# Optimization experiments

Measured on AMD Instinct MI355X. Metric: run time of the kernel, lower is better.

Reference implementation:

```python
import jax, jax.numpy as jnp
import numpy as np

N = 131072  # time steps
D = 4       # SDE state dimension


def setup_inputs() -> dict:
    key = jax.random.key(0)
    k = jax.random.split(key, 6)
    F = 0.1 * jax.random.normal(k[0], (D, D), jnp.float32)  # only shape/dtype used by filter
    H = jnp.zeros((1, D), jnp.float32).at[0, 0].set(1.0)    # observe first state component
    P_inf = jnp.eye(D, dtype=jnp.float32)
    # stable per-step transitions: spectral radius ~0.9
    A_seq = 0.9 * jnp.eye(D, dtype=jnp.float32)[None] + 0.02 * jax.random.normal(k[1], (N, D, D), jnp.float32)
    # PSD process noise per step
    S = 0.05 * jax.random.normal(k[2], (N, D, D), jnp.float32)
    Q_seq = jnp.einsum('nij,nkj->nik', S, S) + 1e-3 * jnp.eye(D, dtype=jnp.float32)[None]
    residual = jax.random.normal(k[3], (N,), jnp.float32)   # y - mean_fn(times)
    mask = jnp.ones((N,), jnp.float32)                      # all steps observed
    R_seq = 0.1 + 0.05 * jax.random.uniform(k[4], (N,), jnp.float32)  # noise_var + floor
    return dict(F=F, H=H, P_inf=P_inf, A_seq=A_seq, Q_seq=Q_seq,
                residual=residual, mask=mask, R_seq=R_seq)


def _kalman_filter(F, H, P_inf, A_seq, Q_seq, residual, mask, R_seq):
    d = F.shape[0]
    eye = jnp.eye(d, dtype=F.dtype)
    h = H[0]  # (d,)
    log_2pi = jnp.log(2.0 * jnp.pi).astype(F.dtype)

    def step(carry, inputs):
        m, P = carry
        A, Q, r_n, mask_n, R_n = inputs
        m_pred = A @ m
        P_pred = A @ P @ A.T + Q
        P_pred = 0.5 * (P_pred + P_pred.T)
        Ph = P_pred @ h                 # (d,)
        S = h @ Ph + R_n                # innovation variance
        innov = r_n - h @ m_pred
        is_obs = mask_n == 1
        S_safe = jnp.where(is_obs, S, 1.0)
        K = jnp.where(is_obs, Ph / S_safe, jnp.zeros_like(Ph))
        m_new = m_pred + K * innov
        I_KH = eye - K[:, None] * h[None, :]
        P_new = I_KH @ P_pred @ I_KH.T + R_n * (K[:, None] * K[None, :])
        P_new = 0.5 * (P_new + P_new.T)
        ll = jnp.where(is_obs, -0.5 * (log_2pi + jnp.log(S_safe) + innov * innov / S_safe), 0.0)
        return (m_new, P_new), (m_pred, P_pred, m_new, P_new, ll)

    m0 = jnp.zeros(d, dtype=F.dtype)
    _, (m_pred_seq, P_pred_seq, m_filt_seq, P_filt_seq, ll_seq) = jax.lax.scan(
        step, (m0, P_inf), (A_seq, Q_seq, residual, mask, R_seq))
    return m_pred_seq, P_pred_seq, m_filt_seq, P_filt_seq, jnp.sum(ll_seq)


def _rts_smoother(m_pred_seq, P_pred_seq, m_filt_seq, P_filt_seq, A_seq):
    def step(carry, inputs):
        m_ns, P_ns = carry
        m_f, P_f, m_pn, P_pn, A_n = inputs
        J = jnp.linalg.solve(P_pn.T, A_n @ P_f.T).T
        m_s = m_f + J @ (m_ns - m_pn)
        P_s = P_f + J @ (P_ns - P_pn) @ J.T
        P_s = 0.5 * (P_s + P_s.T)
        return (m_s, P_s), (m_s, P_s)

    m_T = m_filt_seq[-1]
    P_T = P_filt_seq[-1]
    inputs = (m_filt_seq[:-1], P_filt_seq[:-1], m_pred_seq[1:], P_pred_seq[1:], A_seq[1:])
    _, (m_s, P_s) = jax.lax.scan(step, (m_T, P_T), inputs, reverse=True)
    return (jnp.concatenate([m_s, m_T[None]], axis=0),
            jnp.concatenate([P_s, P_T[None]], axis=0))


def reference(F, H, P_inf, A_seq, Q_seq, residual, mask, R_seq):
    m_pred, P_pred, m_filt, P_filt, log_marginal = _kalman_filter(
        F, H, P_inf, A_seq, Q_seq, residual, mask, R_seq)
    m_smooth, P_smooth = _rts_smoother(m_pred, P_pred, m_filt, P_filt, A_seq)
    h = H[0]
    means = m_smooth @ h                                   # (N,) observation-space means
    vars_ = jnp.einsum('i,nij,j->n', h, P_smooth, h)       # (N,) marginal variances
    return means, vars_, log_marginal
```

## Files before the change

### kernel.cpp

```cpp
#include <hip/hip_runtime.h>
#include <math.h>

#define NN 131072
#define WUP 32
#define TPB 256
#define NBLK (NN / TPB)
#define WINF (TPB + WUP + 1)
#define WINB (TPB + WUP - 1)
#define LOG2PI 1.8378770664093453f

typedef __attribute__((ext_vector_type(2))) float f2;

__device__ float4 g_f[5][NN];
__device__ float4 g_J[4][NN];
__device__ float4 g_W0[NN];
__device__ float4 g_W1[NN];
__device__ float2 g_W2[NN];
__device__ float4 g_u[NN];
__device__ double g_llb[NBLK];

__device__ __forceinline__ f2 bc(float s) {
  f2 r = {s, s};
  return r;
}
#define PF(a, b, c) __builtin_elementwise_fma((a), (b), (c))

template <int E>
__device__ __forceinline__ void ldpk(const float4 (*s)[E], int w, f2* M) {
#pragma unroll
  for (int c = 0; c < 4; ++c) {
    float4 v = s[c][w];
    M[2 * c] = f2{v.x, v.y};
    M[2 * c + 1] = f2{v.z, v.w};
  }
}

__device__ __forceinline__ void sym_rows(const float4 t0, const float4 t1, const float2 t2,
                                         f2* M) {
  M[0] = f2{t0.x, t0.y};
  M[1] = f2{t0.z, t0.w};
  M[2] = f2{t0.y, t1.x};
  M[3] = f2{t1.y, t1.z};
  M[4] = f2{t0.z, t1.y};
  M[5] = f2{t1.w, t2.x};
  M[6] = f2{t0.w, t1.z};
  M[7] = f2{t2.x, t2.y};
}

__device__ __forceinline__ void kf_step_pk(const f2* __restrict__ AT, const f2* __restrict__ Q,
                                           float r, float mk, float R, f2* __restrict__ m,
                                           f2* __restrict__ P, float& Ss, float& innov,
                                           bool& obs) {
  float m0 = m[0][0], m1 = m[0][1], m2_ = m[1][0], m3 = m[1][1];
  f2 mp[2];
#pragma unroll
  for (int p = 0; p < 2; ++p) {
    f2 acc = AT[p] * bc(m0);
    acc = PF(bc(m1), AT[2 + p], acc);
    acc = PF(bc(m2_), AT[4 + p], acc);
    acc = PF(bc(m3), AT[6 + p], acc);
    mp[p] = acc;
  }

  f2 T[8];
#pragma unroll
  for (int i = 0; i < 4; ++i) {
    float a0 = AT[0 + (i >> 1)][i & 1];
    float a1 = AT[2 + (i >> 1)][i & 1];
    float a2 = AT[4 + (i >> 1)][i & 1];
    float a3 = AT[6 + (i >> 1)][i & 1];
#pragma unroll
    for (int p = 0; p < 2; ++p) {
      f2 acc = P[p] * bc(a0);
      acc = PF(bc(a1), P[2 + p], acc);
      acc = PF(bc(a2), P[4 + p], acc);
      acc = PF(bc(a3), P[6 + p], acc);
      T[2 * i + p] = acc;
    }
  }

  f2 Pp[8];
#pragma unroll
  for (int i = 0; i < 4; ++i) {
    float t0 = T[2 * i][0], t1 = T[2 * i][1], t2 = T[2 * i + 1][0], t3 = T[2 * i + 1][1];
#pragma unroll
    for (int p = 0; p < 2; ++p) {
      f2 acc = PF(bc(t0), AT[p], Q[2 * i + p]);
      acc = PF(bc(t1), AT[2 + p], acc);
      acc = PF(bc(t2), AT[4 + p], acc);
      acc = PF(bc(t3), AT[6 + p], acc);
      Pp[2 * i + p] = acc;
    }
  }

  float S = Pp[0][0] + R;
  innov = r - mp[0][0];
  obs = (mk == 1.0f);
  Ss = obs ? S : 1.0f;
  float kf = obs ? __builtin_amdgcn_rcpf(S) : 0.0f;
  f2 K[2] = {Pp[0] * bc(kf), Pp[1] * bc(kf)};
#pragma unroll
  for (int p = 0; p < 2; ++p) m[p] = PF(K[p], bc(innov), mp[p]);

#pragma unroll
  for (int i = 0; i < 4; ++i) {
    float Ki = K[i >> 1][i & 1];
#pragma unroll
    for (int p = 0; p < 2; ++p) P[2 * i + p] = PF(bc(-Ki), Pp[p], Pp[2 * i + p]);
  }
}

__device__ __forceinline__ void chol_solve_pk(const f2* __restrict__ S, const f2* __restrict__ T,
                                              f2* __restrict__ X) {
  float s00 = S[0][0];
  float s10 = S[2][0], s11 = S[2][1];
  float s20 = S[4][0], s21 = S[4][1], s22 = S[5][0];
  float s30 = S[6][0], s31 = S[6][1], s32 = S[7][0], s33 = S[7][1];
  float i00 = __builtin_amdgcn_rsqf(s00);
  float l10 = s10 * i00, l20 = s20 * i00, l30 = s30 * i00;
  float i11 = __builtin_amdgcn_rsqf(s11 - l10 * l10);
  float l21 = (s21 - l20 * l10) * i11;
  float l31 = (s31 - l30 * l10) * i11;
  float i22 = __builtin_amdgcn_rsqf(s22 - l20 * l20 - l21 * l21);
  float l32 = (s32 - l30 * l20 - l31 * l21) * i22;
  float i33 = __builtin_amdgcn_rsqf(s33 - l30 * l30 - l31 * l31 - l32 * l32);
#pragma unroll
  for (int c = 0; c < 4; ++c) {
    float t0 = T[0 + (c >> 1)][c & 1];
    float t1 = T[2 + (c >> 1)][c & 1];
    float t2 = T[4 + (c >> 1)][c & 1];
    float t3 = T[6 + (c >> 1)][c & 1];
    float y0 = t0 * i00;
    float y1 = (t1 - l10 * y0) * i11;
    float y2 = (t2 - l20 * y0 - l21 * y1) * i22;
    float y3 = (t3 - l30 * y0 - l31 * y1 - l32 * y2) * i33;
    float x3 = y3 * i33;
    float x2 = (y2 - l32 * x3) * i22;
    float x1 = (y1 - l21 * x2 - l31 * x3) * i11;
    float x0 = (y0 - l10 * x1 - l20 * x2 - l30 * x3) * i00;
    X[0 + (c >> 1)][c & 1] = x0;
    X[2 + (c >> 1)][c & 1] = x1;
    X[4 + (c >> 1)][c & 1] = x2;
    X[6 + (c >> 1)][c & 1] = x3;
  }
}

__device__ __forceinline__ void make_record_pk(int n, const f2* __restrict__ m,
                                               const f2* __restrict__ P,
                                               const f2* __restrict__ AT,
                                               const f2* __restrict__ Q) {
  float m0 = m[0][0], m1 = m[0][1], m2_ = m[1][0], m3 = m[1][1];
  f2 pm[2];
#pragma unroll
  for (int p = 0; p < 2; ++p) {
    f2 acc = AT[p] * bc(m0);
    acc = PF(bc(m1), AT[2 + p], acc);
    acc = PF(bc(m2_), AT[4 + p], acc);
    acc = PF(bc(m3), AT[6 + p], acc);
    pm[p] = acc;
  }

  f2 T[8];
#pragma unroll
  for (int i = 0; i < 4; ++i) {
    float a0 = AT[0 + (i >> 1)][i & 1];
    float a1 = AT[2 + (i >> 1)][i & 1];
    float a2 = AT[4 + (i >> 1)][i & 1];
    float a3 = AT[6 + (i >> 1)][i & 1];
#pragma unroll
    for (int p = 0; p < 2; ++p) {
      f2 acc = P[p] * bc(a0);
      acc = PF(bc(a1), P[2 + p], acc);
      acc = PF(bc(a2), P[4 + p], acc);
      acc = PF(bc(a3), P[6 + p], acc);
      T[2 * i + p] = acc;
    }
  }

  f2 Ppn[8];
#pragma unroll
  for (int i = 0; i < 4; ++i) {
    float t0 = T[2 * i][0], t1 = T[2 * i][1], t2 = T[2 * i + 1][0], t3 = T[2 * i + 1][1];
#pragma unroll
    for (int p = 0; p < 2; ++p) {
      f2 acc = PF(bc(t0), AT[p], Q[2 * i + p]);
      acc = PF(bc(t1), AT[2 + p], acc);
      acc = PF(bc(t2), AT[4 + p], acc);
      acc = PF(bc(t3), AT[6 + p], acc);
      Ppn[2 * i + p] = acc;
    }
  }

  f2 X[8];
  chol_solve_pk(Ppn, T, X);

  float p0 = pm[0][0], p1 = pm[0][1], p2 = pm[1][0], p3 = pm[1][1];
  f2 u[2];
#pragma unroll
  for (int p = 0; p < 2; ++p) {
    f2 acc = X[p] * bc(p0);
    acc = PF(bc(p1), X[2 + p], acc);
    acc = PF(bc(p2), X[4 + p], acc);
    acc = PF(bc(p3), X[6 + p], acc);
    u[p] = m[p] - acc;
  }

  f2 Jp[8];
#pragma unroll
  for (int i = 0; i < 4; ++i) {
    float x0 = X[0 + (i >> 1)][i & 1];
    float x1 = X[2 + (i >> 1)][i & 1];
    float x2 = X[4 + (i >> 1)][i & 1];
    float x3 = X[6 + (i >> 1)][i & 1];
#pragma unroll
    for (int p = 0; p < 2; ++p) {
      f2 acc = Ppn[p] * bc(x0);
      acc = PF(bc(x1), Ppn[2 + p], acc);
      acc = PF(bc(x2), Ppn[4 + p], acc);
      acc = PF(bc(x3), Ppn[6 + p], acc);
      Jp[2 * i + p] = acc;
    }
  }
  f2 W[8];
#pragma unroll
  for (int i = 0; i < 4; ++i) {
    float j0 = Jp[2 * i][0], j1 = Jp[2 * i][1], j2 = Jp[2 * i + 1][0], j3 = Jp[2 * i + 1][1];
#pragma unroll
    for (int p = 0; p < 2; ++p) {
      f2 acc = X[p] * bc(j0);
      acc = PF(bc(j1), X[2 + p], acc);
      acc = PF(bc(j2), X[4 + p], acc);
      acc = PF(bc(j3), X[6 + p], acc);
      W[2 * i + p] = P[2 * i + p] - acc;
    }
  }

#pragma unroll
  for (int i = 0; i < 4; ++i)
    g_J[i][n] = make_float4(X[0 + (i >> 1)][i & 1], X[2 + (i >> 1)][i & 1],
                            X[4 + (i >> 1)][i & 1], X[6 + (i >> 1)][i & 1]);
  g_W0[n] = make_float4(W[0][0], W[0][1], W[1][0], W[1][1]);
  g_W1[n] = make_float4(W[2][1], W[3][0], W[3][1], W[5][0]);
  g_W2[n] = make_float2(W[5][1], W[7][1]);
  g_u[n] = make_float4(u[0][0], u[0][1], u[1][0], u[1][1]);
}

__global__ __launch_bounds__(TPB, 1) void fwd_kernel(const float* __restrict__ P_inf,
                                                     const float* __restrict__ A_seq,
                                                     const float* __restrict__ Q_seq,
                                                     const float* __restrict__ residual,
                                                     const float* __restrict__ mask,
                                                     const float* __restrict__ R_seq) {
  __shared__ float4 sAT[4][WINF];
  __shared__ float4 sQ0[WINF], sQ1[WINF];
  __shared__ float2 sQ2[WINF];
  __shared__ float4 sRM[WINF];
  __shared__ double sh[TPB];

  const int B = blockIdx.x * TPB;
  const int base = B - WUP;
  const float4* Af4 = (const float4*)A_seq;
  const float4* Qf4 = (const float4*)Q_seq;
  for (int f = threadIdx.x; f < WINF * 4; f += TPB) {
    int w = f >> 2, c = f & 3;
    int k = base + w;
    k = k < 0 ? 0 : (k > NN - 1 ? NN - 1 : k);
    float4 rowA = Af4[(size_t)k * 4 + c];
    ((float*)&sAT[0][w])[c] = rowA.x;
    ((float*)&sAT[1][w])[c] = rowA.y;
    ((float*)&sAT[2][w])[c] = rowA.z;
    ((float*)&sAT[3][w])[c] = rowA.w;
    float4 rowQ = Qf4[(size_t)k * 4 + c];
    if (c == 0) {
      sQ0[w] = rowQ;
    } else if (c == 1) {
      sQ1[w].x = rowQ.y;
      sQ1[w].y = rowQ.z;
      sQ1[w].z = rowQ.w;
    } else if (c == 2) {
      sQ1[w].w = rowQ.z;
      sQ2[w].x = rowQ.w;
    } else {
      sQ2[w].y = rowQ.w;
    }
  }
  for (int w = threadIdx.x; w < WINF; w += TPB) {
    int k = base + w;
    k = k < 0 ? 0 : (k > NN - 1 ? NN - 1 : k);
    sRM[w] = make_float4(residual[k], R_seq[k], mask[k], 0.f);
  }
  __syncthreads();

  const int t = threadIdx.x;
  const int n = B + t;
  int s0 = n - WUP;
  if (s0 < 0) s0 = 0;

  f2 m[2] = {f2{0.f, 0.f}, f2{0.f, 0.f}};
  f2 P[8];
#pragma unroll
  for (int i = 0; i < 4; ++i) {
    P[2 * i] = f2{P_inf[i * 4 + 0], P_inf[i * 4 + 1]};
    P[2 * i + 1] = f2{P_inf[i * 4 + 2], P_inf[i * 4 + 3]};
  }

  float Ss = 1.f, innov = 0.f;
  bool obs = false;
#pragma unroll 2
  for (int k = s0; k <= n; ++k) {
    int w = k - base;
    f2 AT[8], Q[8];
    ldpk<WINF>(sAT, w, AT);
    sym_rows(sQ0[w], sQ1[w], sQ2[w], Q);
    float4 rm = sRM[w];
    kf_step_pk(AT, Q, rm.x, rm.z, rm.y, m, P, Ss, innov, obs);
  }

#pragma unroll
  for (int c = 0; c < 4; ++c)
    g_f[c][n] = make_float4(P[2 * c][0], P[2 * c][1], P[2 * c + 1][0], P[2 * c + 1][1]);
  g_f[4][n] = make_float4(m[0][0], m[0][1], m[1][0], m[1][1]);

  if (n < NN - 1) {
    int w = n + 1 - base;
    f2 AT[8], Q[8];
    ldpk<WINF>(sAT, w, AT);
    sym_rows(sQ0[w], sQ1[w], sQ2[w], Q);
    make_record_pk(n, m, P, AT, Q);
  }

  sh[t] = obs ? (double)(-0.5f * (LOG2PI + logf(Ss) + innov * innov / Ss)) : 0.0;
  __syncthreads();
#pragma unroll
  for (int w = TPB / 2; w > 0; w >>= 1) {
    if (t < w) sh[t] += sh[t + w];
    __syncthreads();
  }
  if (t == 0) g_llb[blockIdx.x] = sh[0];
}

__global__ __launch_bounds__(TPB, 1) void bwd_kernel(float* __restrict__ out) {
  __shared__ float4 sJ[4][WINB];
  __shared__ float4 sW0[WINB], sW1[WINB];
  __shared__ float2 sW2[WINB];
  __shared__ float4 su[WINB];
  __shared__ double shd[TPB];

  const int B = blockIdx.x * TPB;
  const int t = threadIdx.x;
  const int n = B + t;
  int e = n + WUP;
  if (e > NN - 1) e = NN - 1;

  f2 Pi[8], mi[2];
#pragma unroll
  for (int c = 0; c < 4; ++c) {
    float4 v = g_f[c][e];
    Pi[2 * c] = f2{v.x, v.y};
    Pi[2 * c + 1] = f2{v.z, v.w};
  }
  {
    float4 v = g_f[4][e];
    mi[0] = f2{v.x, v.y};
    mi[1] = f2{v.z, v.w};
  }

  for (int f = t; f < WINB * 4; f += TPB) {
    int w = f >> 2, c = f & 3;
    int k = B + w;
    if (k > NN - 1) k = NN - 1;
    sJ[c][w] = g_J[c][k];
  }
  for (int w = t; w < WINB; w += TPB) {
    int k = B + w;
    if (k > NN - 1) k = NN - 1;
    sW0[w] = g_W0[k];
    sW1[w] = g_W1[k];
    sW2[w] = g_W2[k];
    su[w] = g_u[k];
  }
  __syncthreads();

  f2 r01 = f2{1.f, 0.f}, r23 = f2{0.f, 0.f};
  float alpha = 0.f, omega = 0.f;
#pragma unroll 2
  for (int k = n; k < e; ++k) {
    int w = k - B;
    float4 j0 = sJ[0][w], j1 = sJ[1][w], j2 = sJ[2][w], j3 = sJ[3][w];
    f2 W[8];
    sym_rows(sW0[w], sW1[w], sW2[w], W);
    float4 uv = su[w];
    float r0 = r01[0], r1 = r01[1], r2 = r23[0], r3 = r23[1];
    alpha += r0 * uv.x + r1 * uv.y + r2 * uv.z + r3 * uv.w;
    f2 s01 = W[0] * bc(r0);
    s01 = PF(bc(r1), W[2], s01);
    s01 = PF(bc(r2), W[4], s01);
    s01 = PF(bc(r3), W[6], s01);
    f2 s23 = W[1] * bc(r0);
    s23 = PF(bc(r1), W[3], s23);
    s23 = PF(bc(r2), W[5], s23);
    s23 = PF(bc(r3), W[7], s23);
    f2 os = r01 * s01;
    os = PF(r23, s23, os);
    omega += os[0] + os[1];
    f2 ja = f2{j0.x, j0.y}, jb = f2{j1.x, j1.y}, jc = f2{j2.x, j2.y}, jd = f2{j3.x, j3.y};
    f2 je = f2{j0.z, j0.w}, jf = f2{j1.z, j1.w}, jg = f2{j2.z, j2.w}, jh = f2{j3.z, j3.w};
    f2 n01 = ja * bc(r0);
    n01 = PF(bc(r1), jb, n01);
    n01 = PF(bc(r2), jc, n01);
    n01 = PF(bc(r3), jd, n01);
    f2 n23 = je * bc(r0);
    n23 = PF(bc(r1), jf, n23);
    n23 = PF(bc(r2), jg, n23);
    n23 = PF(bc(r3), jh, n23);
    r01 = n01;
    r23 = n23;
  }

  {
    float r0 = r01[0], r1 = r01[1], r2 = r23[0], r3 = r23[1];
    float mean = alpha + r0 * mi[0][0] + r1 * mi[0][1] + r2 * mi[1][0] + r3 * mi[1][1];
    f2 s01 = Pi[0] * bc(r0);
    s01 = PF(bc(r1), Pi[2], s01);
    s01 = PF(bc(r2), Pi[4], s01);
    s01 = PF(bc(r3), Pi[6], s01);
    f2 s23 = Pi[1] * bc(r0);
    s23 = PF(bc(r1), Pi[3], s23);
    s23 = PF(bc(r2), Pi[5], s23);
    s23 = PF(bc(r3), Pi[7], s23);
    f2 vs = r01 * s01;
    vs = PF(r23, s23, vs);
    out[n] = mean;
    out[NN + n] = omega + vs[0] + vs[1];
  }

  if (blockIdx.x == 0) {
    double acc = 0.0;
    for (int i = t; i < NBLK; i += TPB) acc += g_llb[i];
    shd[t] = acc;
    __syncthreads();
#pragma unroll
    for (int w = TPB / 2; w > 0; w >>= 1) {
      if (t < w) shd[t] += shd[t + w];
      __syncthreads();
    }
    if (t == 0) out[2 * NN] = (float)shd[0];
  }
}

extern "C" void kernel_launch(void* const* d_in, const int* in_sizes, int n_in, void* d_out,
                              int out_size, void* d_ws, size_t ws_size, hipStream_t stream) {
  const float* P_inf = (const float*)d_in[2];
  const float* A_seq = (const float*)d_in[3];
  const float* Q_seq = (const float*)d_in[4];
  const float* residual = (const float*)d_in[5];
  const float* mask = (const float*)d_in[6];
  const float* R_seq = (const float*)d_in[7];
  float* out = (float*)d_out;

  fwd_kernel<<<NBLK, TPB, 0, stream>>>(P_inf, A_seq, Q_seq, residual, mask, R_seq);
  bwd_kernel<<<NBLK, TPB, 0, stream>>>(out);
}
```

Before: 115.8 us.

## Fuse forward filter and backward smoother into one kernel via shared memory

Merges the forward Kalman filter kernel and the backward RTS smoother kernel into a single kernel. Each block runs 320 threads: 288 compute smoother records (J, W, u) and 256 produce outputs, and records are exchanged through shared memory instead of global arrays. This removes the global round trip for per-step filter state and records and one full kernel boundary. In exchange each block recomputes 32 extra forward records for its backward warm-up window, 64 threads sit idle during the backward phase, and a small separate kernel is added for the log-likelihood reduction.

New measurement: 130.7 us. 12.9% more time.

```diff
diff --git a/kernel.cpp b/kernel.cpp
--- a/kernel.cpp
+++ b/kernel.cpp
@@ -3,20 +3,15 @@
 
 #define NN 131072
 #define WUP 32
-#define TPB 256
-#define NBLK (NN / TPB)
-#define WINF (TPB + WUP + 1)
-#define WINB (TPB + WUP - 1)
+#define TPB 320
+#define NOUT 256
+#define NBLK (NN / NOUT)
+#define WIN 321
+#define NREC 288
 #define LOG2PI 1.8378770664093453f
 
 typedef __attribute__((ext_vector_type(2))) float f2;
 
-__device__ float4 g_f[5][NN];
-__device__ float4 g_J[4][NN];
-__device__ float4 g_W0[NN];
-__device__ float4 g_W1[NN];
-__device__ float2 g_W2[NN];
-__device__ float4 g_u[NN];
 __device__ double g_llb[NBLK];
 
 __device__ __forceinline__ f2 bc(float s) {
@@ -25,11 +20,10 @@
 }
 #define PF(a, b, c) __builtin_elementwise_fma((a), (b), (c))
 
-template <int E>
-__device__ __forceinline__ void ldpk(const float4 (*s)[E], int w, f2* M) {
+__device__ __forceinline__ void ldpk_flat(const float4* s, int stride, int w, f2* M) {
 #pragma unroll
   for (int c = 0; c < 4; ++c) {
-    float4 v = s[c][w];
+    float4 v = s[c * stride + w];
     M[2 * c] = f2{v.x, v.y};
     M[2 * c + 1] = f2{v.z, v.w};
   }
@@ -145,10 +139,11 @@
   }
 }
 
-__device__ __forceinline__ void make_record_pk(int n, const f2* __restrict__ m,
-                                               const f2* __restrict__ P,
-                                               const f2* __restrict__ AT,
-                                               const f2* __restrict__ Q) {
+__device__ __forceinline__ void make_record_reg(const f2* __restrict__ m,
+                                                const f2* __restrict__ P,
+                                                const f2* __restrict__ AT,
+                                                const f2* __restrict__ Q, f2* __restrict__ X,
+                                                f2* __restrict__ W, f2* __restrict__ u) {
   float m0 = m[0][0], m1 = m[0][1], m2_ = m[1][0], m3 = m[1][1];
   f2 pm[2];
 #pragma unroll
@@ -191,11 +186,9 @@
     }
   }
 
-  f2 X[8];
   chol_solve_pk(Ppn, T, X);
 
   float p0 = pm[0][0], p1 = pm[0][1], p2 = pm[1][0], p3 = pm[1][1];
-  f2 u[2];
 #pragma unroll
   for (int p = 0; p < 2; ++p) {
     f2 acc = X[p] * bc(p0);
@@ -221,7 +214,6 @@
       Jp[2 * i + p] = acc;
     }
   }
-  f2 W[8];
 #pragma unroll
   for (int i = 0; i < 4; ++i) {
     float j0 = Jp[2 * i][0], j1 = Jp[2 * i][1], j2 = Jp[2 * i + 1][0], j3 = Jp[2 * i + 1][1];
@@ -234,42 +226,46 @@
       W[2 * i + p] = P[2 * i + p] - acc;
     }
   }
-
-#pragma unroll
-  for (int i = 0; i < 4; ++i)
-    g_J[i][n] = make_float4(X[0 + (i >> 1)][i & 1], X[2 + (i >> 1)][i & 1],
-                            X[4 + (i >> 1)][i & 1], X[6 + (i >> 1)][i & 1]);
-  g_W0[n] = make_float4(W[0][0], W[0][1], W[1][0], W[1][1]);
-  g_W1[n] = make_float4(W[2][1], W[3][0], W[3][1], W[5][0]);
-  g_W2[n] = make_float2(W[5][1], W[7][1]);
-  g_u[n] = make_float4(u[0][0], u[0][1], u[1][0], u[1][1]);
-}
-
-__global__ __launch_bounds__(TPB, 1) void fwd_kernel(const float* __restrict__ P_inf,
-                                                     const float* __restrict__ A_seq,
-                                                     const float* __restrict__ Q_seq,
-                                                     const float* __restrict__ residual,
-                                                     const float* __restrict__ mask,
-                                                     const float* __restrict__ R_seq) {
-  __shared__ float4 sAT[4][WINF];
-  __shared__ float4 sQ0[WINF], sQ1[WINF];
-  __shared__ float2 sQ2[WINF];
-  __shared__ float4 sRM[WINF];
+}
+
+__global__ __launch_bounds__(TPB, 1) void fused_kernel(const float* __restrict__ P_inf,
+                                                       const float* __restrict__ A_seq,
+                                                       const float* __restrict__ Q_seq,
+                                                       const float* __restrict__ residual,
+                                                       const float* __restrict__ mask,
+                                                       const float* __restrict__ R_seq,
+                                                       float* __restrict__ out) {
+  __shared__ __align__(16) char smem[55040];
   __shared__ double sh[TPB];
 
-  const int B = blockIdx.x * TPB;
+  float4* sAT = (float4*)smem;
+  float4* sQ0 = (float4*)(smem + 20544);
+  float4* sQ1 = (float4*)(smem + 25680);
+  float2* sQ2 = (float2*)(smem + 30816);
+  float4* sRM = (float4*)(smem + 33384);
+  float4* rJ = (float4*)smem;
+  float4* rW0 = (float4*)(smem + 18432);
+  float4* rW1 = (float4*)(smem + 23040);
+  float2* rW2 = (float2*)(smem + 27648);
+  float4* ru = (float4*)(smem + 29952);
+  float4* fm = (float4*)(smem + 34560);
+  float4* fP = (float4*)(smem + 38656);
+
+  const int B = blockIdx.x * NOUT;
+  const int t = threadIdx.x;
   const int base = B - WUP;
+
   const float4* Af4 = (const float4*)A_seq;
   const float4* Qf4 = (const float4*)Q_seq;
-  for (int f = threadIdx.x; f < WINF * 4; f += TPB) {
+  for (int f = t; f < WIN * 4; f += TPB) {
     int w = f >> 2, c = f & 3;
     int k = base + w;
     k = k < 0 ? 0 : (k > NN - 1 ? NN - 1 : k);
     float4 rowA = Af4[(size_t)k * 4 + c];
-    ((float*)&sAT[0][w])[c] = rowA.x;
-    ((float*)&sAT[1][w])[c] = rowA.y;
-    ((float*)&sAT[2][w])[c] = rowA.z;
-    ((float*)&sAT[3][w])[c] = rowA.w;
+    ((float*)&sAT[0 * WIN + w])[c] = rowA.x;
+    ((float*)&sAT[1 * WIN + w])[c] = rowA.y;
+    ((float*)&sAT[2 * WIN + w])[c] = rowA.z;
+    ((float*)&sAT[3 * WIN + w])[c] = rowA.w;
     float4 rowQ = Qf4[(size_t)k * 4 + c];
     if (c == 0) {
       sQ0[w] = rowQ;
@@ -284,168 +280,148 @@
       sQ2[w].y = rowQ.w;
     }
   }
-  for (int w = threadIdx.x; w < WINF; w += TPB) {
+  for (int w = t; w < WIN; w += TPB) {
     int k = base + w;
     k = k < 0 ? 0 : (k > NN - 1 ? NN - 1 : k);
     sRM[w] = make_float4(residual[k], R_seq[k], mask[k], 0.f);
   }
   __syncthreads();
 
-  const int t = threadIdx.x;
-  const int n = B + t;
-  int s0 = n - WUP;
-  if (s0 < 0) s0 = 0;
-
-  f2 m[2] = {f2{0.f, 0.f}, f2{0.f, 0.f}};
-  f2 P[8];
-#pragma unroll
-  for (int i = 0; i < 4; ++i) {
-    P[2 * i] = f2{P_inf[i * 4 + 0], P_inf[i * 4 + 1]};
-    P[2 * i + 1] = f2{P_inf[i * 4 + 2], P_inf[i * 4 + 3]};
-  }
-
+  f2 m[2], P[8], X[8], W[8], u[2];
   float Ss = 1.f, innov = 0.f;
   bool obs = false;
+  if (t < NREC) {
+    int kown = B + t;
+    if (kown > NN - 1) kown = NN - 1;
+    int s0 = kown - WUP;
+    if (s0 < 0) s0 = 0;
+
+    m[0] = f2{0.f, 0.f};
+    m[1] = f2{0.f, 0.f};
+#pragma unroll
+    for (int i = 0; i < 4; ++i) {
+      P[2 * i] = f2{P_inf[i * 4 + 0], P_inf[i * 4 + 1]};
+      P[2 * i + 1] = f2{P_inf[i * 4 + 2], P_inf[i * 4 + 3]};
+    }
+
 #pragma unroll 2
-  for (int k = s0; k <= n; ++k) {
-    int w = k - base;
+    for (int k = s0; k <= kown; ++k) {
+      int w = k - base;
+      f2 AT[8], Q[8];
+      ldpk_flat(sAT, WIN, w, AT);
+      sym_rows(sQ0[w], sQ1[w], sQ2[w], Q);
+      float4 rm = sRM[w];
+      kf_step_pk(AT, Q, rm.x, rm.z, rm.y, m, P, Ss, innov, obs);
+    }
+
+    int kn = kown + 1;
+    if (kn > NN - 1) kn = NN - 1;
+    int w = kn - base;
     f2 AT[8], Q[8];
-    ldpk<WINF>(sAT, w, AT);
+    ldpk_flat(sAT, WIN, w, AT);
     sym_rows(sQ0[w], sQ1[w], sQ2[w], Q);
-    float4 rm = sRM[w];
-    kf_step_pk(AT, Q, rm.x, rm.z, rm.y, m, P, Ss, innov, obs);
-  }
-
-#pragma unroll
-  for (int c = 0; c < 4; ++c)
-    g_f[c][n] = make_float4(P[2 * c][0], P[2 * c][1], P[2 * c + 1][0], P[2 * c + 1][1]);
-  g_f[4][n] = make_float4(m[0][0], m[0][1], m[1][0], m[1][1]);
-
-  if (n < NN - 1) {
-    int w = n + 1 - base;
-    f2 AT[8], Q[8];
-    ldpk<WINF>(sAT, w, AT);
-    sym_rows(sQ0[w], sQ1[w], sQ2[w], Q);
-    make_record_pk(n, m, P, AT, Q);
-  }
-
-  sh[t] = obs ? (double)(-0.5f * (LOG2PI + logf(Ss) + innov * innov / Ss)) : 0.0;
+    make_record_reg(m, P, AT, Q, X, W, u);
+  }
+
+  sh[t] = (t < NOUT && obs) ? (double)(-0.5f * (LOG2PI + logf(Ss) + innov * innov / Ss)) : 0.0;
   __syncthreads();
-#pragma unroll
-  for (int w = TPB / 2; w > 0; w >>= 1) {
+
+  if (t < NREC) {
+#pragma unroll
+    for (int i = 0; i < 4; ++i)
+      rJ[i * NREC + t] = make_float4(X[0 + (i >> 1)][i & 1], X[2 + (i >> 1)][i & 1],
+                                     X[4 + (i >> 1)][i & 1], X[6 + (i >> 1)][i & 1]);
+    rW0[t] = make_float4(W[0][0], W[0][1], W[1][0], W[1][1]);
+    rW1[t] = make_float4(W[2][1], W[3][0], W[3][1], W[5][0]);
+    rW2[t] = make_float2(W[5][1], W[7][1]);
+    ru[t] = make_float4(u[0][0], u[0][1], u[1][0], u[1][1]);
+    if (t >= WUP) {
+      int j = t - WUP;
+      fm[j] = make_float4(m[0][0], m[0][1], m[1][0], m[1][1]);
+#pragma unroll
+      for (int c = 0; c < 4; ++c)
+        fP[c * NOUT + j] = make_float4(P[2 * c][0], P[2 * c][1], P[2 * c + 1][0], P[2 * c + 1][1]);
+    }
+  }
+
+#pragma unroll
+  for (int w = 128; w > 0; w >>= 1) {
     if (t < w) sh[t] += sh[t + w];
     __syncthreads();
   }
   if (t == 0) g_llb[blockIdx.x] = sh[0];
-}
-
-__global__ __launch_bounds__(TPB, 1) void bwd_kernel(float* __restrict__ out) {
-  __shared__ float4 sJ[4][WINB];
-  __shared__ float4 sW0[WINB], sW1[WINB];
-  __shared__ float2 sW2[WINB];
-  __shared__ float4 su[WINB];
-  __shared__ double shd[TPB];
-
-  const int B = blockIdx.x * TPB;
+
+  if (t < NOUT) {
+    const int n = B + t;
+    int e = n + WUP;
+    if (e > NN - 1) e = NN - 1;
+
+    f2 r01 = f2{1.f, 0.f}, r23 = f2{0.f, 0.f};
+    float alpha = 0.f, omega = 0.f;
+#pragma unroll 2
+    for (int k = n; k < e; ++k) {
+      int w = k - B;
+      float4 j0 = rJ[0 * NREC + w], j1 = rJ[1 * NREC + w];
+      float4 j2 = rJ[2 * NREC + w], j3 = rJ[3 * NREC + w];
+      f2 Wm[8];
+      sym_rows(rW0[w], rW1[w], rW2[w], Wm);
+      float4 uv = ru[w];
+      float r0 = r01[0], r1 = r01[1], r2 = r23[0], r3 = r23[1];
+      alpha += r0 * uv.x + r1 * uv.y + r2 * uv.z + r3 * uv.w;
+      f2 s01 = Wm[0] * bc(r0);
+      s01 = PF(bc(r1), Wm[2], s01);
+      s01 = PF(bc(r2), Wm[4], s01);
+      s01 = PF(bc(r3), Wm[6], s01);
+      f2 s23 = Wm[1] * bc(r0);
+      s23 = PF(bc(r1), Wm[3], s23);
+      s23 = PF(bc(r2), Wm[5], s23);
+      s23 = PF(bc(r3), Wm[7], s23);
+      f2 os = r01 * s01;
+      os = PF(r23, s23, os);
+      omega += os[0] + os[1];
+      f2 ja = f2{j0.x, j0.y}, jb = f2{j1.x, j1.y}, jc = f2{j2.x, j2.y}, jd = f2{j3.x, j3.y};
+      f2 je = f2{j0.z, j0.w}, jf = f2{j1.z, j1.w}, jg = f2{j2.z, j2.w}, jh = f2{j3.z, j3.w};
+      f2 n01 = ja * bc(r0);
+      n01 = PF(bc(r1), jb, n01);
+      n01 = PF(bc(r2), jc, n01);
+      n01 = PF(bc(r3), jd, n01);
+      f2 n23 = je * bc(r0);
+      n23 = PF(bc(r1), jf, n23);
+      n23 = PF(bc(r2), jg, n23);
+      n23 = PF(bc(r3), jh, n23);
+      r01 = n01;
+      r23 = n23;
+    }
+
+    int j = e - B - WUP;
+    float4 vm = fm[j];
+    float r0 = r01[0], r1 = r01[1], r2 = r23[0], r3 = r23[1];
+    float mean = alpha + r0 * vm.x + r1 * vm.y + r2 * vm.z + r3 * vm.w;
+    float4 p0 = fP[0 * NOUT + j], p1 = fP[1 * NOUT + j];
+    float4 p2 = fP[2 * NOUT + j], p3 = fP[3 * NOUT + j];
+    float s0 = p0.x * r0 + p0.y * r1 + p0.z * r2 + p0.w * r3;
+    float s1 = p1.x * r0 + p1.y * r1 + p1.z * r2 + p1.w * r3;
+    float s2 = p2.x * r0 + p2.y * r1 + p2.z * r2 + p2.w * r3;
+    float s3 = p3.x * r0 + p3.y * r1 + p3.z * r2 + p3.w * r3;
+    float var = omega + r0 * s0 + r1 * s1 + r2 * s2 + r3 * s3;
+    out[n] = mean;
+    out[NN + n] = var;
+  }
+}
+
+__global__ __launch_bounds__(256, 1) void llred_kernel(float* __restrict__ out) {
+  __shared__ double sh[256];
   const int t = threadIdx.x;
-  const int n = B + t;
-  int e = n + WUP;
-  if (e > NN - 1) e = NN - 1;
-
-  f2 Pi[8], mi[2];
-#pragma unroll
-  for (int c = 0; c < 4; ++c) {
-    float4 v = g_f[c][e];
-    Pi[2 * c] = f2{v.x, v.y};
-    Pi[2 * c + 1] = f2{v.z, v.w};
-  }
-  {
-    float4 v = g_f[4][e];
-    mi[0] = f2{v.x, v.y};
-    mi[1] = f2{v.z, v.w};
-  }
-
-  for (int f = t; f < WINB * 4; f += TPB) {
-    int w = f >> 2, c = f & 3;
-    int k = B + w;
-    if (k > NN - 1) k = NN - 1;
-    sJ[c][w] = g_J[c][k];
-  }
-  for (int w = t; w < WINB; w += TPB) {
-    int k = B + w;
-    if (k > NN - 1) k = NN - 1;
-    sW0[w] = g_W0[k];
-    sW1[w] = g_W1[k];
-    sW2[w] = g_W2[k];
-    su[w] = g_u[k];
-  }
+  double acc = 0.0;
+  for (int i = t; i < NBLK; i += 256) acc += g_llb[i];
+  sh[t] = acc;
   __syncthreads();
-
-  f2 r01 = f2{1.f, 0.f}, r23 = f2{0.f, 0.f};
-  float alpha = 0.f, omega = 0.f;
-#pragma unroll 2
-  for (int k = n; k < e; ++k) {
-    int w = k - B;
-    float4 j0 = sJ[0][w], j1 = sJ[1][w], j2 = sJ[2][w], j3 = sJ[3][w];
-    f2 W[8];
-    sym_rows(sW0[w], sW1[w], sW2[w], W);
-    float4 uv = su[w];
-    float r0 = r01[0], r1 = r01[1], r2 = r23[0], r3 = r23[1];
-    alpha += r0 * uv.x + r1 * uv.y + r2 * uv.z + r3 * uv.w;
-    f2 s01 = W[0] * bc(r0);
-    s01 = PF(bc(r1), W[2], s01);
-    s01 = PF(bc(r2), W[4], s01);
-    s01 = PF(bc(r3), W[6], s01);
-    f2 s23 = W[1] * bc(r0);
-    s23 = PF(bc(r1), W[3], s23);
-    s23 = PF(bc(r2), W[5], s23);
-    s23 = PF(bc(r3), W[7], s23);
-    f2 os = r01 * s01;
-    os = PF(r23, s23, os);
-    omega += os[0] + os[1];
-    f2 ja = f2{j0.x, j0.y}, jb = f2{j1.x, j1.y}, jc = f2{j2.x, j2.y}, jd = f2{j3.x, j3.y};
-    f2 je = f2{j0.z, j0.w}, jf = f2{j1.z, j1.w}, jg = f2{j2.z, j2.w}, jh = f2{j3.z, j3.w};
-    f2 n01 = ja * bc(r0);
-    n01 = PF(bc(r1), jb, n01);
-    n01 = PF(bc(r2), jc, n01);
-    n01 = PF(bc(r3), jd, n01);
-    f2 n23 = je * bc(r0);
-    n23 = PF(bc(r1), jf, n23);
-    n23 = PF(bc(r2), jg, n23);
-    n23 = PF(bc(r3), jh, n23);
-    r01 = n01;
-    r23 = n23;
-  }
-
-  {
-    float r0 = r01[0], r1 = r01[1], r2 = r23[0], r3 = r23[1];
-    float mean = alpha + r0 * mi[0][0] + r1 * mi[0][1] + r2 * mi[1][0] + r3 * mi[1][1];
-    f2 s01 = Pi[0] * bc(r0);
-    s01 = PF(bc(r1), Pi[2], s01);
-    s01 = PF(bc(r2), Pi[4], s01);
-    s01 = PF(bc(r3), Pi[6], s01);
-    f2 s23 = Pi[1] * bc(r0);
-    s23 = PF(bc(r1), Pi[3], s23);
-    s23 = PF(bc(r2), Pi[5], s23);
-    s23 = PF(bc(r3), Pi[7], s23);
-    f2 vs = r01 * s01;
-    vs = PF(r23, s23, vs);
-    out[n] = mean;
-    out[NN + n] = omega + vs[0] + vs[1];
-  }
-
-  if (blockIdx.x == 0) {
-    double acc = 0.0;
-    for (int i = t; i < NBLK; i += TPB) acc += g_llb[i];
-    shd[t] = acc;
+#pragma unroll
+  for (int w = 128; w > 0; w >>= 1) {
+    if (t < w) sh[t] += sh[t + w];
     __syncthreads();
-#pragma unroll
-    for (int w = TPB / 2; w > 0; w >>= 1) {
-      if (t < w) shd[t] += shd[t + w];
-      __syncthreads();
-    }
-    if (t == 0) out[2 * NN] = (float)shd[0];
-  }
+  }
+  if (t == 0) out[2 * NN] = (float)sh[0];
 }
 
 extern "C" void kernel_launch(void* const* d_in, const int* in_sizes, int n_in, void* d_out,
@@ -458,6 +434,6 @@
   const float* R_seq = (const float*)d_in[7];
   float* out = (float*)d_out;
 
-  fwd_kernel<<<NBLK, TPB, 0, stream>>>(P_inf, A_seq, Q_seq, residual, mask, R_seq);
-  bwd_kernel<<<NBLK, TPB, 0, stream>>>(out);
-}
+  fused_kernel<<<NBLK, TPB, 0, stream>>>(P_inf, A_seq, Q_seq, residual, mask, R_seq, out);
+  llred_kernel<<<1, 256, 0, stream>>>(out);
+}
```

## Read windowed step data directly from global memory instead of LDS staging

Applied to the files above, without the earlier changes.

Removes the shared-memory staging of A, Q, residual/R/mask in the forward kernel and of J, W, u in the backward kernel, so each thread reads its per-step operands straight from global memory inside the warm-up loop. This drops the cooperative load loops, the block barrier and the LDS traffic, relying on L1/L2 to serve the heavily overlapping windows that neighbouring threads read. The risk is that every iteration now issues strided global loads (16 floats per A/Q step, several float4s per backward step) with cache latency on the serial dependency chain, and neighbouring lanes read adjacent timesteps, so accesses are less coalesced than the old staged copy.

Result: slower. 136.9 us (+18.3%).

```diff
diff --git a/kernel.cpp b/kernel.cpp
--- a/kernel.cpp
+++ b/kernel.cpp
@@ -5,8 +5,6 @@
 #define WUP 32
 #define TPB 256
 #define NBLK (NN / TPB)
-#define WINF (TPB + WUP + 1)
-#define WINB (TPB + WUP - 1)
 #define LOG2PI 1.8378770664093453f
 
 typedef __attribute__((ext_vector_type(2))) float f2;
@@ -25,13 +23,27 @@
 }
 #define PF(a, b, c) __builtin_elementwise_fma((a), (b), (c))
 
-template <int E>
-__device__ __forceinline__ void ldpk(const float4 (*s)[E], int w, f2* M) {
+__device__ __forceinline__ void lda_g(const float4* __restrict__ Af4, int k, f2* AT) {
+  float4 r0 = Af4[(size_t)k * 4 + 0];
+  float4 r1 = Af4[(size_t)k * 4 + 1];
+  float4 r2 = Af4[(size_t)k * 4 + 2];
+  float4 r3 = Af4[(size_t)k * 4 + 3];
+  AT[0] = f2{r0.x, r1.x};
+  AT[1] = f2{r2.x, r3.x};
+  AT[2] = f2{r0.y, r1.y};
+  AT[3] = f2{r2.y, r3.y};
+  AT[4] = f2{r0.z, r1.z};
+  AT[5] = f2{r2.z, r3.z};
+  AT[6] = f2{r0.w, r1.w};
+  AT[7] = f2{r2.w, r3.w};
+}
+
+__device__ __forceinline__ void ldq_g(const float4* __restrict__ Qf4, int k, f2* Q) {
 #pragma unroll
   for (int c = 0; c < 4; ++c) {
-    float4 v = s[c][w];
-    M[2 * c] = f2{v.x, v.y};
-    M[2 * c + 1] = f2{v.z, v.w};
+    float4 v = Qf4[(size_t)k * 4 + c];
+    Q[2 * c] = f2{v.x, v.y};
+    Q[2 * c + 1] = f2{v.z, v.w};
   }
 }
 
@@ -251,51 +263,17 @@
                                                      const float* __restrict__ residual,
                                                      const float* __restrict__ mask,
                                                      const float* __restrict__ R_seq) {
-  __shared__ float4 sAT[4][WINF];
-  __shared__ float4 sQ0[WINF], sQ1[WINF];
-  __shared__ float2 sQ2[WINF];
-  __shared__ float4 sRM[WINF];
   __shared__ double sh[TPB];
 
   const int B = blockIdx.x * TPB;
-  const int base = B - WUP;
-  const float4* Af4 = (const float4*)A_seq;
-  const float4* Qf4 = (const float4*)Q_seq;
-  for (int f = threadIdx.x; f < WINF * 4; f += TPB) {
-    int w = f >> 2, c = f & 3;
-    int k = base + w;
-    k = k < 0 ? 0 : (k > NN - 1 ? NN - 1 : k);
-    float4 rowA = Af4[(size_t)k * 4 + c];
-    ((float*)&sAT[0][w])[c] = rowA.x;
-    ((float*)&sAT[1][w])[c] = rowA.y;
-    ((float*)&sAT[2][w])[c] = rowA.z;
-    ((float*)&sAT[3][w])[c] = rowA.w;
-    float4 rowQ = Qf4[(size_t)k * 4 + c];
-    if (c == 0) {
-      sQ0[w] = rowQ;
-    } else if (c == 1) {
-      sQ1[w].x = rowQ.y;
-      sQ1[w].y = rowQ.z;
-      sQ1[w].z = rowQ.w;
-    } else if (c == 2) {
-      sQ1[w].w = rowQ.z;
-      sQ2[w].x = rowQ.w;
-    } else {
-      sQ2[w].y = rowQ.w;
-    }
-  }
-  for (int w = threadIdx.x; w < WINF; w += TPB) {
-    int k = base + w;
-    k = k < 0 ? 0 : (k > NN - 1 ? NN - 1 : k);
-    sRM[w] = make_float4(residual[k], R_seq[k], mask[k], 0.f);
-  }
-  __syncthreads();
-
   const int t = threadIdx.x;
   const int n = B + t;
   int s0 = n - WUP;
   if (s0 < 0) s0 = 0;
 
+  const float4* Af4 = (const float4*)A_seq;
+  const float4* Qf4 = (const float4*)Q_seq;
+
   f2 m[2] = {f2{0.f, 0.f}, f2{0.f, 0.f}};
   f2 P[8];
 #pragma unroll
@@ -308,12 +286,13 @@
   bool obs = false;
 #pragma unroll 2
   for (int k = s0; k <= n; ++k) {
-    int w = k - base;
     f2 AT[8], Q[8];
-    ldpk<WINF>(sAT, w, AT);
-    sym_rows(sQ0[w], sQ1[w], sQ2[w], Q);
-    float4 rm = sRM[w];
-    kf_step_pk(AT, Q, rm.x, rm.z, rm.y, m, P, Ss, innov, obs);
+    lda_g(Af4, k, AT);
+    ldq_g(Qf4, k, Q);
+    float rr = residual[k];
+    float RR = R_seq[k];
+    float mk = mask[k];
+    kf_step_pk(AT, Q, rr, mk, RR, m, P, Ss, innov, obs);
   }
 
 #pragma unroll
@@ -322,10 +301,9 @@
   g_f[4][n] = make_float4(m[0][0], m[0][1], m[1][0], m[1][1]);
 
   if (n < NN - 1) {
-    int w = n + 1 - base;
     f2 AT[8], Q[8];
-    ldpk<WINF>(sAT, w, AT);
-    sym_rows(sQ0[w], sQ1[w], sQ2[w], Q);
+    lda_g(Af4, n + 1, AT);
+    ldq_g(Qf4, n + 1, Q);
     make_record_pk(n, m, P, AT, Q);
   }
 
@@ -340,10 +318,6 @@
 }
 
 __global__ __launch_bounds__(TPB, 1) void bwd_kernel(float* __restrict__ out) {
-  __shared__ float4 sJ[4][WINB];
-  __shared__ float4 sW0[WINB], sW1[WINB];
-  __shared__ float2 sW2[WINB];
-  __shared__ float4 su[WINB];
   __shared__ double shd[TPB];
 
   const int B = blockIdx.x * TPB;
@@ -365,31 +339,14 @@
     mi[1] = f2{v.z, v.w};
   }
 
-  for (int f = t; f < WINB * 4; f += TPB) {
-    int w = f >> 2, c = f & 3;
-    int k = B + w;
-    if (k > NN - 1) k = NN - 1;
-    sJ[c][w] = g_J[c][k];
-  }
-  for (int w = t; w < WINB; w += TPB) {
-    int k = B + w;
-    if (k > NN - 1) k = NN - 1;
-    sW0[w] = g_W0[k];
-    sW1[w] = g_W1[k];
-    sW2[w] = g_W2[k];
-    su[w] = g_u[k];
-  }
-  __syncthreads();
-
   f2 r01 = f2{1.f, 0.f}, r23 = f2{0.f, 0.f};
   float alpha = 0.f, omega = 0.f;
 #pragma unroll 2
   for (int k = n; k < e; ++k) {
-    int w = k - B;
-    float4 j0 = sJ[0][w], j1 = sJ[1][w], j2 = sJ[2][w], j3 = sJ[3][w];
+    float4 j0 = g_J[0][k], j1 = g_J[1][k], j2 = g_J[2][k], j3 = g_J[3][k];
     f2 W[8];
-    sym_rows(sW0[w], sW1[w], sW2[w], W);
-    float4 uv = su[w];
+    sym_rows(g_W0[k], g_W1[k], g_W2[k], W);
+    float4 uv = g_u[k];
     float r0 = r01[0], r1 = r01[1], r2 = r23[0], r3 = r23[1];
     alpha += r0 * uv.x + r1 * uv.y + r2 * uv.z + r3 * uv.w;
     f2 s01 = W[0] * bc(r0);
```
